# Optimization experiments

Measured on AMD Instinct MI355X. Metric: run time of the kernel, lower is better.

## Reference

```python
import jax, jax.numpy as jnp
import numpy as np

N_POINTS = 64
N_DIM = 2 * N_POINTS          # 128
N_CONTROL = 2
FC = [1024, 1024]
DT = 0.1
ELEMS_A = 4 * N_POINTS        # 256 (computed but unused, matching original)
ELEMS_B = N_DIM * N_CONTROL   # 256


def setup_inputs() -> dict:
    key = jax.random.key(0)
    ks = jax.random.split(key, 8)
    B, T = 4096, 64
    states = jax.random.normal(ks[0], (B, T, N_DIM), dtype=jnp.float32)
    actions = jax.random.normal(ks[1], (B, T, N_CONTROL), dtype=jnp.float32)
    d_in = N_DIM + N_CONTROL  # 130
    scale = lambda fan_in: 1.0 / np.sqrt(fan_in)
    W1 = jax.random.normal(ks[2], (d_in, FC[0]), dtype=jnp.float32) * scale(d_in)
    b1 = jnp.zeros((FC[0],), dtype=jnp.float32)
    W2 = jax.random.normal(ks[3], (FC[0], FC[1]), dtype=jnp.float32) * scale(FC[0])
    b2 = jnp.zeros((FC[1],), dtype=jnp.float32)
    W3 = jax.random.normal(ks[4], (FC[1], ELEMS_A + ELEMS_B), dtype=jnp.float32) * scale(FC[1])
    b3 = jnp.zeros((ELEMS_A + ELEMS_B,), dtype=jnp.float32)
    return {"states": states, "actions": actions,
            "W1": W1, "b1": b1, "W2": W2, "b2": b2, "W3": W3, "b3": b3}


def reference(states, actions, W1, b1, W2, b2, W3, b3):
    # states: [B, T, n_dim], actions: [B, T, 2]
    s0 = states[:, 0]  # [B, n_dim]
    actions_t = jnp.swapaxes(actions, 0, 1)  # [T, B, 2]

    def step(s, a):
        z = jnp.concatenate([s, a], axis=1)          # [B, n_dim+2]
        z = jax.nn.relu(z @ W1 + b1)
        z = jax.nn.relu(z @ W2 + b2)
        params = z @ W3 + b3                          # [B, elems_A + elems_B]
        # A_t params (params[:, :ELEMS_A]) are computed but unused in the original update.
        B_params = params[:, ELEMS_A:]                # [B, 4*n_points]
        Bmat = B_params.reshape(-1, N_DIM, N_CONTROL) # block rows: [B, 2*n_points, 2]
        s_next = s + jnp.einsum('bnc,bc->bn', Bmat, a) * DT
        return s_next, s_next

    _, traj = jax.lax.scan(step, s0, actions_t)       # traj: [T, B, n_dim]
    gen = jnp.concatenate([s0[:, None], jnp.swapaxes(traj, 0, 1)], axis=1)
    return gen  # [B, T+1, n_dim]
```

## Files before the change

### kernel.cpp

```cpp
#include <hip/hip_runtime.h>
#include <stdint.h>

#define B_SZ 4096
#define T_SZ 64
#define ND   128
#define HID  1024
#define PO   256

typedef __attribute__((ext_vector_type(8))) short bf16x8;
typedef __attribute__((ext_vector_type(4))) float f32x4;

__device__ __forceinline__ unsigned short f2bf(float x) {
  unsigned int u = __float_as_uint(x);
  u += 0x7fffu + ((u >> 16) & 1u);
  return (unsigned short)(u >> 16);
}
__device__ __forceinline__ float bf2f(unsigned short h) {
  return __uint_as_float(((unsigned int)h) << 16);
}

__device__ __forceinline__ void g2lds(const void* g, void* l) {
  __builtin_amdgcn_global_load_lds(
      (const __attribute__((address_space(1))) unsigned int*)g,
      (__attribute__((address_space(3))) unsigned int*)l, 16, 0, 0);
}

template <int BM, int BN, int MT, int NT, int EPI>
__global__ __launch_bounds__(256, 1) void gemm_split(
    const unsigned short* __restrict__ Ahi, const unsigned short* __restrict__ Alo,
    const unsigned short* __restrict__ Bhi, const unsigned short* __restrict__ Blo,
    const float* __restrict__ bias, int K, int ldc,
    const float* __restrict__ a_t, const float* __restrict__ w1r,
    unsigned short* __restrict__ Zhi, unsigned short* __restrict__ Zlo,
    float* __restrict__ Pout) {
  constexpr int BK = 32;
  static_assert(BM == BN, "square tiles only");
  constexpr int RA = (BM * BK * 2) / 4096;
  __shared__ __attribute__((aligned(16))) unsigned short AsH[BM * BK];
  __shared__ __attribute__((aligned(16))) unsigned short AsL[BM * BK];
  __shared__ __attribute__((aligned(16))) unsigned short BsH[BN * BK];
  __shared__ __attribute__((aligned(16))) unsigned short BsL[BN * BK];

  const int tid  = threadIdx.x;
  const int lane = tid & 63;
  const int wave = tid >> 6;
  const int wm = (wave >> 1) * (MT * 16);
  const int wn = (wave & 1) * (NT * 16);
  const int m0 = blockIdx.x * BM;
  const int n0 = blockIdx.y * BN;
  const size_t Kb = (size_t)K * 2;

  size_t gA[RA], gB[RA];
  int lL[RA];
#pragma unroll
  for (int r = 0; r < RA; ++r) {
    int L = (r * 256 + tid) * 16;
    int row = L >> 6;
    int colb = L & 63;
    lL[r] = L;
    gA[r] = (size_t)(m0 + row) * Kb + colb;
    gB[r] = (size_t)(n0 + row) * Kb + colb;
  }

  f32x4 acc[MT][NT] = {};
  const char* Ah = (const char*)Ahi;
  const char* Al = (const char*)Alo;
  const char* Bh = (const char*)Bhi;
  const char* Bl = (const char*)Blo;
  char* asH = (char*)AsH; char* asL = (char*)AsL;
  char* bsH = (char*)BsH; char* bsL = (char*)BsL;

  const int kIt = K / BK;
  for (int it = 0; it < kIt; ++it) {
    const size_t kadd = (size_t)it * (BK * 2);
#pragma unroll
    for (int r = 0; r < RA; ++r) {
      g2lds(Ah + gA[r] + kadd, asH + lL[r]);
      g2lds(Al + gA[r] + kadd, asL + lL[r]);
      g2lds(Bh + gB[r] + kadd, bsH + lL[r]);
      g2lds(Bl + gB[r] + kadd, bsL + lL[r]);
    }
    __syncthreads();

    bf16x8 fa_h[MT], fa_l[MT], fb_h[NT], fb_l[NT];
#pragma unroll
    for (int mt = 0; mt < MT; ++mt) {
      int off = (wm + mt * 16 + (lane & 15)) * BK + (lane >> 4) * 8;
      fa_h[mt] = *(const bf16x8*)&AsH[off];
      fa_l[mt] = *(const bf16x8*)&AsL[off];
    }
#pragma unroll
    for (int nt = 0; nt < NT; ++nt) {
      int off = (wn + nt * 16 + (lane & 15)) * BK + (lane >> 4) * 8;
      fb_h[nt] = *(const bf16x8*)&BsH[off];
      fb_l[nt] = *(const bf16x8*)&BsL[off];
    }
#pragma unroll
    for (int mt = 0; mt < MT; ++mt)
#pragma unroll
      for (int nt = 0; nt < NT; ++nt) {
        acc[mt][nt] = __builtin_amdgcn_mfma_f32_16x16x32_bf16(fa_h[mt], fb_h[nt], acc[mt][nt], 0, 0, 0);
        acc[mt][nt] = __builtin_amdgcn_mfma_f32_16x16x32_bf16(fa_l[mt], fb_h[nt], acc[mt][nt], 0, 0, 0);
        acc[mt][nt] = __builtin_amdgcn_mfma_f32_16x16x32_bf16(fa_h[mt], fb_l[nt], acc[mt][nt], 0, 0, 0);
      }
    __syncthreads();
  }

#pragma unroll
  for (int mt = 0; mt < MT; ++mt) {
    const int mb = m0 + wm + mt * 16 + ((lane >> 4) << 2);
    float a0v[4], a1v[4];
    if (EPI == 1) {
#pragma unroll
      for (int r = 0; r < 4; ++r) {
        a0v[r] = a_t[(mb + r) * 2];
        a1v[r] = a_t[(mb + r) * 2 + 1];
      }
    }
#pragma unroll
    for (int nt = 0; nt < NT; ++nt) {
      const int n = n0 + wn + nt * 16 + (lane & 15);
      const float bv = bias[n];
      float w0 = 0.f, w1 = 0.f;
      if (EPI == 1) { w0 = w1r[n]; w1 = w1r[HID + n]; }
#pragma unroll
      for (int r = 0; r < 4; ++r) {
        float v = acc[mt][nt][r] + bv;
        if (EPI == 1) v += a0v[r] * w0 + a1v[r] * w1;
        const size_t idx = (size_t)(mb + r) * ldc + n;
        if (EPI == 0) {
          Pout[idx] = v;
        } else {
          v = fmaxf(v, 0.f);
          unsigned short h = f2bf(v);
          Zhi[idx] = h;
          Zlo[idx] = f2bf(v - bf2f(h));
        }
      }
    }
  }
}

__global__ void prep_kernel(
    const float* __restrict__ states, const float* __restrict__ actions,
    const float* __restrict__ W1, const float* __restrict__ W2,
    const float* __restrict__ W3,
    unsigned short* __restrict__ W1tH, unsigned short* __restrict__ W1tL,
    unsigned short* __restrict__ W2tH, unsigned short* __restrict__ W2tL,
    unsigned short* __restrict__ W3tH, unsigned short* __restrict__ W3tL,
    float* __restrict__ aT, float* __restrict__ s,
    unsigned short* __restrict__ sH, unsigned short* __restrict__ sL,
    float* __restrict__ gen) {
  const int tid = blockIdx.x * blockDim.x + threadIdx.x;
  const int stride = gridDim.x * blockDim.x;
  for (int i = tid; i < ND * HID; i += stride) {
    int k = i >> 10, j = i & 1023;
    float v = W1[i];
    unsigned short h = f2bf(v);
    W1tH[j * ND + k] = h;
    W1tL[j * ND + k] = f2bf(v - bf2f(h));
  }
  for (int i = tid; i < HID * HID; i += stride) {
    int k = i >> 10, j = i & 1023;
    float v = W2[i];
    unsigned short h = f2bf(v);
    W2tH[j * HID + k] = h;
    W2tL[j * HID + k] = f2bf(v - bf2f(h));
  }
  for (int i = tid; i < HID * PO; i += stride) {
    int k = i >> 8, j = i & 255;
    float v = W3[k * 512 + 256 + j];
    unsigned short h = f2bf(v);
    W3tH[j * HID + k] = h;
    W3tL[j * HID + k] = f2bf(v - bf2f(h));
  }
  for (int i = tid; i < B_SZ * T_SZ; i += stride) {
    int b = i >> 6, t = i & 63;
    float2 v = ((const float2*)actions)[i];
    ((float2*)aT)[t * B_SZ + b] = v;
  }
  for (int i = tid; i < B_SZ * ND; i += stride) {
    int b = i >> 7, n = i & 127;
    float v = states[(size_t)b * (T_SZ * ND) + n];
    s[i] = v;
    unsigned short h = f2bf(v);
    sH[i] = h;
    sL[i] = f2bf(v - bf2f(h));
    gen[(size_t)b * ((T_SZ + 1) * ND) + n] = v;
  }
}

__global__ void update_kernel(const float* __restrict__ P, const float* __restrict__ a_t,
                              float* __restrict__ s, unsigned short* __restrict__ sH,
                              unsigned short* __restrict__ sL, float* __restrict__ gen,
                              int t) {
  int i = blockIdx.x * 256 + threadIdx.x;
  int b = i >> 7, n = i & 127;
  float2 p = ((const float2*)P)[(size_t)b * 128 + n];
  float a0 = a_t[b * 2], a1 = a_t[b * 2 + 1];
  float v = s[i] + (p.x * a0 + p.y * a1) * 0.1f;
  s[i] = v;
  unsigned short h = f2bf(v);
  sH[i] = h;
  sL[i] = f2bf(v - bf2f(h));
  gen[(size_t)b * ((T_SZ + 1) * ND) + (size_t)(t + 1) * ND + n] = v;
}

extern "C" void kernel_launch(void* const* d_in, const int* in_sizes, int n_in,
                              void* d_out, int out_size, void* d_ws, size_t ws_size,
                              hipStream_t stream) {
  const float* states  = (const float*)d_in[0];
  const float* actions = (const float*)d_in[1];
  const float* W1 = (const float*)d_in[2];
  const float* b1 = (const float*)d_in[3];
  const float* W2 = (const float*)d_in[4];
  const float* b2 = (const float*)d_in[5];
  const float* W3 = (const float*)d_in[6];
  const float* b3 = (const float*)d_in[7];
  float* gen = (float*)d_out;

  char* w = (char*)d_ws;
  float*          s    = (float*)(w + 0);
  unsigned short* sH   = (unsigned short*)(w + (2ull << 20));
  unsigned short* sL   = (unsigned short*)(w + (3ull << 20));
  unsigned short* z1H  = (unsigned short*)(w + (4ull << 20));
  unsigned short* z1L  = (unsigned short*)(w + (12ull << 20));
  unsigned short* z2H  = (unsigned short*)(w + (20ull << 20));
  unsigned short* z2L  = (unsigned short*)(w + (28ull << 20));
  float*          P    = (float*)(w + (36ull << 20));
  float*          aT   = (float*)(w + (40ull << 20));
  unsigned short* W1tH = (unsigned short*)(w + (42ull << 20));
  unsigned short* W1tL = (unsigned short*)(w + (42ull << 20) + 262144);
  unsigned short* W2tH = (unsigned short*)(w + (43ull << 20));
  unsigned short* W2tL = (unsigned short*)(w + (45ull << 20));
  unsigned short* W3tH = (unsigned short*)(w + (47ull << 20));
  unsigned short* W3tL = (unsigned short*)(w + (47ull << 20) + 524288);

  prep_kernel<<<2048, 256, 0, stream>>>(states, actions, W1, W2, W3,
      W1tH, W1tL, W2tH, W2tL, W3tH, W3tL, aT, s, sH, sL, gen);

  const float* w1r = W1 + 128 * 1024;
  for (int t = 0; t < 64; ++t) {
    const float* at = aT + (size_t)t * B_SZ * 2;
    gemm_split<128, 128, 4, 4, 1><<<dim3(32, 8), 256, 0, stream>>>(
        sH, sL, W1tH, W1tL, b1, 128, HID, at, w1r, z1H, z1L, (float*)nullptr);
    gemm_split<128, 128, 4, 4, 2><<<dim3(32, 8), 256, 0, stream>>>(
        z1H, z1L, W2tH, W2tL, b2, HID, HID, (const float*)nullptr,
        (const float*)nullptr, z2H, z2L, (float*)nullptr);
    gemm_split<64, 64, 2, 2, 0><<<dim3(64, 4), 256, 0, stream>>>(
        z2H, z2L, W3tH, W3tL, b3 + 256, HID, PO, (const float*)nullptr,
        (const float*)nullptr, (unsigned short*)nullptr, (unsigned short*)nullptr, P);
    update_kernel<<<2048, 256, 0, stream>>>(P, at, s, sH, sL, gen, t);
  }
}
```

Measured before the change: 5.487 ms.

## Double-buffer LDS tiles in split-bf16 GEMM and fuse state update into layer-3 epilogue

The GEMM main loop now double-buffers the A/B LDS tiles. It issues the global-to-LDS loads for the next K slice before computing on the current one, and drops the second barrier per iteration. The separate update kernel and the P scratch buffer are removed. The third GEMM's epilogue pairs adjacent output columns with a lane shuffle and writes the new state, its hi/lo bf16 split and the gen row directly. This cuts one launch and one global round trip per timestep, at the cost of twice the LDS per block. It also relies on the async LDS loads being complete by the next barrier.

```diff
diff --git a/kernel.cpp b/kernel.cpp
--- a/kernel.cpp
+++ b/kernel.cpp
@@ -32,14 +32,15 @@
     const float* __restrict__ bias, int K, int ldc,
     const float* __restrict__ a_t, const float* __restrict__ w1r,
     unsigned short* __restrict__ Zhi, unsigned short* __restrict__ Zlo,
-    float* __restrict__ Pout) {
+    float* __restrict__ S, float* __restrict__ gen, int t) {
   constexpr int BK = 32;
   static_assert(BM == BN, "square tiles only");
   constexpr int RA = (BM * BK * 2) / 4096;
-  __shared__ __attribute__((aligned(16))) unsigned short AsH[BM * BK];
-  __shared__ __attribute__((aligned(16))) unsigned short AsL[BM * BK];
-  __shared__ __attribute__((aligned(16))) unsigned short BsH[BN * BK];
-  __shared__ __attribute__((aligned(16))) unsigned short BsL[BN * BK];
+  constexpr int TB = BM * BK * 2;
+  __shared__ __attribute__((aligned(16))) unsigned short AsH[2][BM * BK];
+  __shared__ __attribute__((aligned(16))) unsigned short AsL[2][BM * BK];
+  __shared__ __attribute__((aligned(16))) unsigned short BsH[2][BN * BK];
+  __shared__ __attribute__((aligned(16))) unsigned short BsL[2][BN * BK];
 
   const int tid  = threadIdx.x;
   const int lane = tid & 63;
@@ -71,29 +72,43 @@
   char* bsH = (char*)BsH; char* bsL = (char*)BsL;
 
   const int kIt = K / BK;
+
+#pragma unroll
+  for (int r = 0; r < RA; ++r) {
+    g2lds(Ah + gA[r], asH + lL[r]);
+    g2lds(Al + gA[r], asL + lL[r]);
+    g2lds(Bh + gB[r], bsH + lL[r]);
+    g2lds(Bl + gB[r], bsL + lL[r]);
+  }
+
+  int cur = 0;
   for (int it = 0; it < kIt; ++it) {
-    const size_t kadd = (size_t)it * (BK * 2);
-#pragma unroll
-    for (int r = 0; r < RA; ++r) {
-      g2lds(Ah + gA[r] + kadd, asH + lL[r]);
-      g2lds(Al + gA[r] + kadd, asL + lL[r]);
-      g2lds(Bh + gB[r] + kadd, bsH + lL[r]);
-      g2lds(Bl + gB[r] + kadd, bsL + lL[r]);
-    }
     __syncthreads();
+
+    if (it + 1 < kIt) {
+      const size_t kadd = (size_t)(it + 1) * (BK * 2);
+      const int lb = (cur ^ 1) * TB;
+#pragma unroll
+      for (int r = 0; r < RA; ++r) {
+        g2lds(Ah + gA[r] + kadd, asH + lb + lL[r]);
+        g2lds(Al + gA[r] + kadd, asL + lb + lL[r]);
+        g2lds(Bh + gB[r] + kadd, bsH + lb + lL[r]);
+        g2lds(Bl + gB[r] + kadd, bsL + lb + lL[r]);
+      }
+    }
 
     bf16x8 fa_h[MT], fa_l[MT], fb_h[NT], fb_l[NT];
 #pragma unroll
     for (int mt = 0; mt < MT; ++mt) {
       int off = (wm + mt * 16 + (lane & 15)) * BK + (lane >> 4) * 8;
-      fa_h[mt] = *(const bf16x8*)&AsH[off];
-      fa_l[mt] = *(const bf16x8*)&AsL[off];
+      fa_h[mt] = *(const bf16x8*)&AsH[cur][off];
+      fa_l[mt] = *(const bf16x8*)&AsL[cur][off];
     }
 #pragma unroll
     for (int nt = 0; nt < NT; ++nt) {
       int off = (wn + nt * 16 + (lane & 15)) * BK + (lane >> 4) * 8;
-      fb_h[nt] = *(const bf16x8*)&BsH[off];
-      fb_l[nt] = *(const bf16x8*)&BsL[off];
+      fb_h[nt] = *(const bf16x8*)&BsH[cur][off];
+      fb_l[nt] = *(const bf16x8*)&BsL[cur][off];
     }
 #pragma unroll
     for (int mt = 0; mt < MT; ++mt)
@@ -103,14 +118,14 @@
         acc[mt][nt] = __builtin_amdgcn_mfma_f32_16x16x32_bf16(fa_l[mt], fb_h[nt], acc[mt][nt], 0, 0, 0);
         acc[mt][nt] = __builtin_amdgcn_mfma_f32_16x16x32_bf16(fa_h[mt], fb_l[nt], acc[mt][nt], 0, 0, 0);
       }
-    __syncthreads();
+    cur ^= 1;
   }
 
 #pragma unroll
   for (int mt = 0; mt < MT; ++mt) {
     const int mb = m0 + wm + mt * 16 + ((lane >> 4) << 2);
     float a0v[4], a1v[4];
-    if (EPI == 1) {
+    if (EPI == 1 || EPI == 3) {
 #pragma unroll
       for (int r = 0; r < 4; ++r) {
         a0v[r] = a_t[(mb + r) * 2];
@@ -126,13 +141,23 @@
 #pragma unroll
       for (int r = 0; r < 4; ++r) {
         float v = acc[mt][nt][r] + bv;
-        if (EPI == 1) v += a0v[r] * w0 + a1v[r] * w1;
-        const size_t idx = (size_t)(mb + r) * ldc + n;
-        if (EPI == 0) {
-          Pout[idx] = v;
+        if (EPI == 3) {
+          float vx = __shfl_xor(v, 1);
+          if (!(lane & 1)) {
+            const int b = mb + r;
+            const int j = n >> 1;
+            const float sv = S[b * ND + j] + (v * a0v[r] + vx * a1v[r]) * 0.1f;
+            S[b * ND + j] = sv;
+            unsigned short h = f2bf(sv);
+            Zhi[b * ND + j] = h;
+            Zlo[b * ND + j] = f2bf(sv - bf2f(h));
+            gen[(size_t)b * ((T_SZ + 1) * ND) + (size_t)(t + 1) * ND + j] = sv;
+          }
         } else {
+          if (EPI == 1) v += a0v[r] * w0 + a1v[r] * w1;
           v = fmaxf(v, 0.f);
           unsigned short h = f2bf(v);
+          const size_t idx = (size_t)(mb + r) * ldc + n;
           Zhi[idx] = h;
           Zlo[idx] = f2bf(v - bf2f(h));
         }
@@ -190,22 +215,6 @@
   }
 }
 
-__global__ void update_kernel(const float* __restrict__ P, const float* __restrict__ a_t,
-                              float* __restrict__ s, unsigned short* __restrict__ sH,
-                              unsigned short* __restrict__ sL, float* __restrict__ gen,
-                              int t) {
-  int i = blockIdx.x * 256 + threadIdx.x;
-  int b = i >> 7, n = i & 127;
-  float2 p = ((const float2*)P)[(size_t)b * 128 + n];
-  float a0 = a_t[b * 2], a1 = a_t[b * 2 + 1];
-  float v = s[i] + (p.x * a0 + p.y * a1) * 0.1f;
-  s[i] = v;
-  unsigned short h = f2bf(v);
-  sH[i] = h;
-  sL[i] = f2bf(v - bf2f(h));
-  gen[(size_t)b * ((T_SZ + 1) * ND) + (size_t)(t + 1) * ND + n] = v;
-}
-
 extern "C" void kernel_launch(void* const* d_in, const int* in_sizes, int n_in,
                               void* d_out, int out_size, void* d_ws, size_t ws_size,
                               hipStream_t stream) {
@@ -227,7 +236,6 @@
   unsigned short* z1L  = (unsigned short*)(w + (12ull << 20));
   unsigned short* z2H  = (unsigned short*)(w + (20ull << 20));
   unsigned short* z2L  = (unsigned short*)(w + (28ull << 20));
-  float*          P    = (float*)(w + (36ull << 20));
   float*          aT   = (float*)(w + (40ull << 20));
   unsigned short* W1tH = (unsigned short*)(w + (42ull << 20));
   unsigned short* W1tL = (unsigned short*)(w + (42ull << 20) + 262144);
@@ -243,13 +251,13 @@
   for (int t = 0; t < 64; ++t) {
     const float* at = aT + (size_t)t * B_SZ * 2;
     gemm_split<128, 128, 4, 4, 1><<<dim3(32, 8), 256, 0, stream>>>(
-        sH, sL, W1tH, W1tL, b1, 128, HID, at, w1r, z1H, z1L, (float*)nullptr);
+        sH, sL, W1tH, W1tL, b1, 128, HID, at, w1r, z1H, z1L,
+        (float*)nullptr, (float*)nullptr, 0);
     gemm_split<128, 128, 4, 4, 2><<<dim3(32, 8), 256, 0, stream>>>(
         z1H, z1L, W2tH, W2tL, b2, HID, HID, (const float*)nullptr,
-        (const float*)nullptr, z2H, z2L, (float*)nullptr);
-    gemm_split<64, 64, 2, 2, 0><<<dim3(64, 4), 256, 0, stream>>>(
-        z2H, z2L, W3tH, W3tL, b3 + 256, HID, PO, (const float*)nullptr,
-        (const float*)nullptr, (unsigned short*)nullptr, (unsigned short*)nullptr, P);
-    update_kernel<<<2048, 256, 0, stream>>>(P, at, s, sH, sL, gen, t);
-  }
-}
+        (const float*)nullptr, z2H, z2L, (float*)nullptr, (float*)nullptr, 0);
+    gemm_split<64, 64, 2, 2, 3><<<dim3(64, 4), 256, 0, stream>>>(
+        z2H, z2L, W3tH, W3tL, b3 + 256, HID, PO, at, (const float*)nullptr,
+        sH, sL, s, gen, t);
+  }
+}
```

Measured after the change: 5.282 ms. -3.7%, faster.
